# Performance work log

Hardware: AMD Instinct MI355X
Metric: run time of the kernel (lower is better)

Reference implementation:

```python
import jax, jax.numpy as jnp
import numpy as np
import math

H = 12   # num_attention_heads
DH = 64  # attention_head_size
D = H * DH  # hidden_size = 768


def _split_heads(x):
    # [b, s, D] -> [b, H, s, DH]
    b, s, _ = x.shape
    return x.reshape(b, s, H, DH).transpose(0, 2, 1, 3)


def setup_inputs() -> dict:
    key = jax.random.key(0)
    ks = jax.random.split(key, 8)
    B, S, G, NUM_CTX = 32, 512, 16, 8
    real_b = B // NUM_CTX
    inp = {
        "hidden_states": jax.random.normal(ks[0], (B, S, D), dtype=jnp.float32),
        "attention_mask": jnp.zeros((B, 1, 1, S), dtype=jnp.float32),
        "global_tokens_embed": jax.random.normal(ks[1], (real_b, G, D), dtype=jnp.float32),
        "Wq": jax.random.normal(ks[2], (D, D), dtype=jnp.float32) * 0.02,
        "bq": jnp.zeros((D,), dtype=jnp.float32),
        "Wk": jax.random.normal(ks[3], (D, D), dtype=jnp.float32) * 0.02,
        "bk": jnp.zeros((D,), dtype=jnp.float32),
        "Wv": jax.random.normal(ks[4], (D, D), dtype=jnp.float32) * 0.02,
        "bv": jnp.zeros((D,), dtype=jnp.float32),
        "num_ctx": 8,
    }
    return inp


def reference(hidden_states, attention_mask, global_tokens_embed,
              Wq, bq, Wk, bk, Wv, bv, num_ctx):
    B, S, _ = hidden_states.shape
    real_b = B // num_ctx
    G = global_tokens_embed.shape[1]
    scale = 1.0 / math.sqrt(DH)

    # Q/K/V projections for packed contexts
    q = _split_heads(hidden_states @ Wq + bq)   # [B,H,S,DH]
    k = _split_heads(hidden_states @ Wk + bk)
    v = _split_heads(hidden_states @ Wv + bv)

    # Global token projections
    gq = _split_heads(global_tokens_embed @ Wq + bq)  # [real_b,H,G,DH]
    gk = _split_heads(global_tokens_embed @ Wk + bk)
    gv = _split_heads(global_tokens_embed @ Wv + bv)

    # ---- Global-token cross attention over all contexts of each real batch ----
    # [B,H,S,DH] -> [real_b, H, num_ctx*S, DH]
    full_k = k.transpose(0, 2, 1, 3).reshape(real_b, num_ctx * S, H, DH).transpose(0, 2, 1, 3)
    full_v = v.transpose(0, 2, 1, 3).reshape(real_b, num_ctx * S, H, DH).transpose(0, 2, 1, 3)
    full_k = jnp.concatenate([gk, full_k], axis=2)  # [real_b,H,G+num_ctx*S,DH]
    full_v = jnp.concatenate([gv, full_v], axis=2)

    g_scores = jnp.einsum('bhgd,bhkd->bhgk', gq, full_k) * scale
    g_mask = attention_mask.reshape(real_b, num_ctx * S)[:, None, None, :]
    g_mask = jnp.concatenate([jnp.zeros((real_b, 1, 1, G), g_mask.dtype), g_mask], axis=3)
    g_scores = g_scores + g_mask
    g_probs = jax.nn.softmax(g_scores, axis=-1)
    g_ctx = jnp.einsum('bhgk,bhkd->bhgd', g_probs, full_v)
    g_ctx = g_ctx.transpose(0, 2, 1, 3).reshape(real_b, G, D)  # [real_b,G,D]

    # ---- Local attention: each context attends to its own tokens + global tokens ----
    gk_rep = jnp.broadcast_to(gk[:, None], (real_b, num_ctx, H, G, DH)).reshape(B, H, G, DH)
    gv_rep = jnp.broadcast_to(gv[:, None], (real_b, num_ctx, H, G, DH)).reshape(B, H, G, DH)
    k2 = jnp.concatenate([gk_rep, k], axis=2)  # [B,H,G+S,DH]
    v2 = jnp.concatenate([gv_rep, v], axis=2)
    mask2 = jnp.concatenate([jnp.zeros((B, 1, 1, G), attention_mask.dtype), attention_mask], axis=3)

    scores = jnp.einsum('bhqd,bhkd->bhqk', q, k2) * scale + mask2  # [B,H,S,G+S]
    probs = jax.nn.softmax(scores, axis=-1)
    ctx = jnp.einsum('bhqk,bhkd->bhqd', probs, v2)
    ctx = ctx.transpose(0, 2, 1, 3).reshape(B, S, D)  # [B,S,D]

    return ctx, g_ctx
```

## Files before the change

### kernel.cpp

```cpp
#include <hip/hip_runtime.h>
#include <hip/hip_bf16.h>
#include <stdint.h>

#define NH 12
#define DHD 64
#define DM 768
#define BB 32
#define SS 512
#define GG 16
#define NCTX 8
#define RBATCH 4
#define NSPLIT 16
#define OUTG_OFF ((size_t)BB * SS * DM)

#define XROWS 16512
#define NALL 2304
#define NX8 (XROWS * DM / 8)
#define NB8 (NALL / 8)
#define NM8 (BB * SS / 8)

#define LOG2E 1.4426950408889634f
#define QSCALE 0.18033688011112042f

typedef __bf16 bf16x8 __attribute__((ext_vector_type(8)));
typedef float f32x4 __attribute__((ext_vector_type(4)));
typedef float f32x16 __attribute__((ext_vector_type(16)));

__device__ __forceinline__ float b2f(unsigned short u) {
    union { unsigned int i; float f; } x;
    x.i = ((unsigned int)u) << 16;
    return x.f;
}
__device__ __forceinline__ unsigned short f2b(float f) {
    __hip_bfloat16 h = __float2bfloat16(f);
    return *reinterpret_cast<unsigned short*>(&h);
}
__device__ __forceinline__ unsigned int pk2(float a, float b) {
    return ((unsigned int)f2b(b) << 16) | (unsigned int)f2b(a);
}
__device__ __forceinline__ float ex2(float x) {
    return __builtin_amdgcn_exp2f(x);
}
__device__ __forceinline__ float ldv(const void* p, size_t i, int isf32) {
    return isf32 ? ((const float*)p)[i] : b2f(((const unsigned short*)p)[i]);
}
__device__ __forceinline__ void stv(void* p, size_t i, int isf32, float v) {
    if (isf32) ((float*)p)[i] = v;
    else       ((unsigned short*)p)[i] = f2b(v);
}
__device__ __forceinline__ void async_cp16(const unsigned short* g, unsigned short* l) {
    __builtin_amdgcn_global_load_lds(
        (const __attribute__((address_space(1))) unsigned int*)g,
        (__attribute__((address_space(3))) unsigned int*)l, 16, 0, 0);
}

__device__ __forceinline__ void vt_pair_store(unsigned int* Vt32, int vr, int scc,
                                              uint4 a, uint4 b, int ldq) {
    const unsigned int* au = (const unsigned int*)&a;
    const unsigned int* bu = (const unsigned int*)&b;
    #pragma unroll
    for (int i = 0; i < 4; i++) {
        const int d0 = scc + 2 * i;
        const int swz = ((vr >> 3) ^ ((d0 >> 3) & 7));
        const int i32 = d0 * ldq + (swz << 2) + ((vr & 7) >> 1);
        Vt32[i32]       = __builtin_amdgcn_perm(bu[i], au[i], 0x05040100u);
        Vt32[i32 + ldq] = __builtin_amdgcn_perm(bu[i], au[i], 0x07060302u);
    }
}

__global__ __launch_bounds__(256) void detect_dtype(
    const unsigned short* __restrict__ Wq, int* __restrict__ flag)
{
    __shared__ int hi, zz;
    if (threadIdx.x == 0) { hi = 0; zz = 0; }
    __syncthreads();
    int lh = 0, lz = 0;
    for (int i = threadIdx.x; i < 4096; i += 256) {
        unsigned short u = Wq[2 * i];
        if (((u >> 7) & 0xFF) >= 130) lh++;
        if (u == 0) lz++;
    }
    atomicAdd(&hi, lh);
    atomicAdd(&zz, lz);
    __syncthreads();
    if (threadIdx.x == 0) *flag = (hi > 512 || zz > 3500) ? 1 : 0;
}

__global__ __launch_bounds__(256) void cvt_x(
    const void* __restrict__ hs, const void* __restrict__ gte,
    const void* __restrict__ bq, const void* __restrict__ bk,
    const void* __restrict__ bv, const void* __restrict__ mask,
    const int* __restrict__ flag,
    unsigned short* __restrict__ Xb, unsigned short* __restrict__ b_all,
    unsigned short* __restrict__ wmask)
{
    const int e = blockIdx.x * 256 + threadIdx.x;
    const int isf32 = *flag;
    if (e < NX8) {
        const int base = e * 8;
        const int row = base / DM, col = base % DM;
        unsigned short o8[8];
        if (row < 16384) {
            if (isf32) {
                float4 a = ((const float4*)hs)[e * 2];
                float4 c = ((const float4*)hs)[e * 2 + 1];
                o8[0]=f2b(a.x); o8[1]=f2b(a.y); o8[2]=f2b(a.z); o8[3]=f2b(a.w);
                o8[4]=f2b(c.x); o8[5]=f2b(c.y); o8[6]=f2b(c.z); o8[7]=f2b(c.w);
            } else {
                *(uint4*)o8 = ((const uint4*)hs)[e];
            }
        } else if (row < 16448) {
            size_t soff = (size_t)(row - 16384) * DM + col;
            #pragma unroll
            for (int i = 0; i < 8; i++) o8[i] = f2b(ldv(gte, soff + i, isf32));
        } else {
            #pragma unroll
            for (int i = 0; i < 8; i++) o8[i] = 0;
        }
        *(uint4*)&Xb[base] = *(const uint4*)o8;
    } else if (e < NX8 + NB8) {
        const int i0 = (e - NX8) * 8;
        #pragma unroll
        for (int i = 0; i < 8; i++) {
            int ng = i0 + i;
            int z = ng / DM;
            const void* src = (z == 0) ? bq : (z == 1) ? bk : bv;
            b_all[ng] = f2b(ldv(src, ng % DM, isf32));
        }
    } else if (e < NX8 + NB8 + NM8) {
        const int i0 = (e - NX8 - NB8) * 8;
        #pragma unroll
        for (int i = 0; i < 8; i++)
            wmask[i0 + i] = f2b(ldv(mask, i0 + i, isf32) * LOG2E);
    }
}

__global__ __launch_bounds__(256) void cvt_w(
    const void* __restrict__ Wq, const void* __restrict__ Wk,
    const void* __restrict__ Wv, const int* __restrict__ flag,
    unsigned short* __restrict__ Wt)
{
    __shared__ float T[64][65];
    const int kt = blockIdx.x;
    const int ngt = blockIdx.y;
    const int z = ngt / 12, nt = ngt % 12;
    const int tid = threadIdx.x;
    const int isf32 = *flag;
    const void* W = (z == 0) ? Wq : (z == 1) ? Wk : Wv;

    for (int jj = 0; jj < 16; jj++) {
        int el = tid + jj * 256;
        int r = el >> 6, c = el & 63;
        T[r][c] = ldv(W, (size_t)(kt * 64 + r) * DM + nt * 64 + c, isf32);
    }
    __syncthreads();
    for (int jj = 0; jj < 16; jj++) {
        int el = tid + jj * 256;
        int rn = el >> 6, ck = el & 63;
        Wt[(size_t)(z * DM + nt * 64 + rn) * DM + kt * 64 + ck] = f2b(T[ck][rn]);
    }
}

#define QKV_NWG (129 * 18)
__global__ __launch_bounds__(256) void qkv_gemm(
    const unsigned short* __restrict__ Xb,
    const unsigned short* __restrict__ Wt,
    const unsigned short* __restrict__ b_all,
    unsigned short* __restrict__ q, unsigned short* __restrict__ kk_,
    unsigned short* __restrict__ v,
    unsigned short* __restrict__ gq, unsigned short* __restrict__ gk,
    unsigned short* __restrict__ gv)
{
    __shared__ __align__(16) unsigned short As[2][2][128 * 32];
    __shared__ __align__(16) unsigned short Bs[2][2][128 * 32];

    const int orig = blockIdx.x;
    const int q8 = QKV_NWG >> 3, r8 = QKV_NWG & 7;
    const int xcd = orig & 7, lin = orig >> 3;
    const int swz = (xcd < r8 ? xcd * (q8 + 1) : r8 * (q8 + 1) + (xcd - r8) * q8) + lin;
    const int mt = swz / 18, nt = swz - mt * 18;

    const int tid = threadIdx.x;
    const int wave = tid >> 6, lane = tid & 63;
    const int quad = lane >> 4, l16 = lane & 15;
    const int wm = wave & 1, wn = wave >> 1;
    const int z = nt / 6;
    unsigned short* YL = (z == 0) ? q : (z == 1) ? kk_ : v;
    unsigned short* YG = (z == 0) ? gq : (z == 1) ? gk : gv;
    const float qsc = (z == 0) ? QSCALE : 1.0f;

    const int sr = tid >> 2, sc = (tid & 3) * 8;

    const unsigned short* Arow0 = &Xb[(size_t)(mt * 128 + sr) * DM + sc];
    const unsigned short* Arow1 = Arow0 + (size_t)64 * DM;
    const unsigned short* Brow0 = &Wt[(size_t)(nt * 128 + sr) * DM + sc];
    const unsigned short* Brow1 = Brow0 + (size_t)64 * DM;

    f32x4 acc[4][4];
    #pragma unroll
    for (int i = 0; i < 4; i++)
        for (int j = 0; j < 4; j++)
            for (int r = 0; r < 4; r++) acc[i][j][r] = 0.f;

#define QKV_STAGE_PAIR(p, bb) do {                                       \
        const int k0_ = (p) * 64;                                        \
        async_cp16(Arow0 + k0_,      &As[(bb)][0][wave * 512]);          \
        async_cp16(Arow1 + k0_,      &As[(bb)][0][2048 + wave * 512]);   \
        async_cp16(Brow0 + k0_,      &Bs[(bb)][0][wave * 512]);          \
        async_cp16(Brow1 + k0_,      &Bs[(bb)][0][2048 + wave * 512]);   \
        async_cp16(Arow0 + k0_ + 32, &As[(bb)][1][wave * 512]);          \
        async_cp16(Arow1 + k0_ + 32, &As[(bb)][1][2048 + wave * 512]);   \
        async_cp16(Brow0 + k0_ + 32, &Bs[(bb)][1][wave * 512]);          \
        async_cp16(Brow1 + k0_ + 32, &Bs[(bb)][1][2048 + wave * 512]);   \
    } while (0)

    QKV_STAGE_PAIR(0, 0);
    __syncthreads();

    int cur = 0;
    for (int p = 0; p < 12; p++) {
        if (p < 11) QKV_STAGE_PAIR(p + 1, cur ^ 1);

        #pragma unroll
        for (int sub = 0; sub < 2; sub++) {
            bf16x8 af[4], bf[4];
            #pragma unroll
            for (int ib = 0; ib < 4; ib++)
                af[ib] = *(const bf16x8*)&As[cur][sub][(wm * 64 + ib * 16 + l16) * 32 + quad * 8];
            #pragma unroll
            for (int jb = 0; jb < 4; jb++)
                bf[jb] = *(const bf16x8*)&Bs[cur][sub][(wn * 64 + jb * 16 + l16) * 32 + quad * 8];
            #pragma unroll
            for (int ib = 0; ib < 4; ib++)
                #pragma unroll
                for (int jb = 0; jb < 4; jb++)
                    acc[ib][jb] = __builtin_amdgcn_mfma_f32_16x16x32_bf16(
                        bf[jb], af[ib], acc[ib][jb], 0, 0, 0);
        }

        if (p < 11) __syncthreads();
        cur ^= 1;
    }
#undef QKV_STAGE_PAIR

    #pragma unroll
    for (int ib = 0; ib < 4; ib++) {
        const int m = mt * 128 + wm * 64 + ib * 16 + l16;
        if (m >= 16448) continue;
        const bool loc = (m < 16384);
        const int b = m >> 9, s = m & 511;
        const int gl = m - 16384;
        const int rbx = gl >> 4, g = gl & 15;
        #pragma unroll
        for (int jb = 0; jb < 4; jb++) {
            const int ng0 = nt * 128 + wn * 64 + jb * 16 + quad * 4;
            const int o = ng0 - z * DM;
            const int h = o >> 6, dh0 = o & 63;
            const uint2 bu = *(const uint2*)&b_all[ng0];
            const unsigned short* bp = (const unsigned short*)&bu;
            const float y0 = (acc[ib][jb][0] + b2f(bp[0])) * qsc;
            const float y1 = (acc[ib][jb][1] + b2f(bp[1])) * qsc;
            const float y2 = (acc[ib][jb][2] + b2f(bp[2])) * qsc;
            const float y3 = (acc[ib][jb][3] + b2f(bp[3])) * qsc;
            uint2 o2;
            o2.x = pk2(y0, y1);
            o2.y = pk2(y2, y3);
            if (loc) {
                *(uint2*)&YL[(((size_t)b * NH + h) * SS + s) * DHD + dh0] = o2;
            } else {
                *(uint2*)&YG[(((size_t)rbx * NH + h) * GG + g) * DHD + dh0] = o2;
            }
        }
    }
}

#define AL_NWG (4 * NH * BB)
__global__ __launch_bounds__(256) void attn_local(
    const unsigned short* __restrict__ q,
    const unsigned short* __restrict__ k,
    const unsigned short* __restrict__ v,
    const unsigned short* __restrict__ gk,
    const unsigned short* __restrict__ gv,
    const unsigned short* __restrict__ wmask,
    const int* __restrict__ flag,
    void* __restrict__ out)
{
    __shared__ __align__(16) unsigned short Ks[2][64 * 64];
    __shared__ __align__(16) unsigned short Vt[2][64 * 64];

    const int orig = blockIdx.x;
    const int swz = (orig & 7) * (AL_NWG / 8) + (orig >> 3);
    const int qt = swz & 3;
    const int hb = swz >> 2;
    const int h = hb % NH, b = hb / NH;

    const int rb = b >> 3;
    const int tid = threadIdx.x, wave = tid >> 6, lane = tid & 63;
    const int l31 = lane & 31, h8 = lane >> 5;
    const int isf32 = *flag;
    const int q0 = qt * 128 + wave * 32;

    const size_t bh = (size_t)b * NH + h;
    const unsigned short* qp = q + bh * SS * DHD;
    const unsigned short* kp = k + bh * SS * DHD;
    const unsigned short* vp = v + bh * SS * DHD;
    const size_t gbh = (size_t)rb * NH + h;
    const unsigned short* gkp = gk + gbh * GG * DHD;
    const unsigned short* gvp = gv + gbh * GG * DHD;

    bf16x8 qf[4];
    #pragma unroll
    for (int kb = 0; kb < 4; kb++)
        qf[kb] = *(const bf16x8*)&qp[(size_t)(q0 + l31) * DHD + kb * 16 + h8 * 8];

    f32x16 oacc[2];
    #pragma unroll
    for (int mb = 0; mb < 2; mb++)
        #pragma unroll
        for (int j = 0; j < 16; j++) oacc[mb][j] = 0.f;
    float m_s = -1e30f, l_s = 0.f;

    const int sr = tid >> 3, scc = (tid & 7) * 8;
    const int vr = sr * 2;
    const int agc = (((lane & 7) ^ ((lane >> 3) & 7)) << 3);
    const int arow = 8 * wave + (lane >> 3);

    if (sr < 16) {
        uint4 kx = *(const uint4*)&gkp[sr * DHD + scc];
        *(uint4*)&Ks[0][sr * 64 + (((scc >> 3) ^ (sr & 7)) << 3)] = kx;
    } else {
        uint4 zz4 = {0, 0, 0, 0};
        *(uint4*)&Ks[0][sr * 64 + (((scc >> 3) ^ (sr & 7)) << 3)] = zz4;
    }
    {
        uint4 va0 = {0, 0, 0, 0}, vb0 = {0, 0, 0, 0};
        if (sr < 8) {
            va0 = *(const uint4*)&gvp[vr * DHD + scc];
            vb0 = *(const uint4*)&gvp[(vr + 1) * DHD + scc];
        }
        vt_pair_store((unsigned int*)Vt[0], vr, scc, va0, vb0, 32);
    }
    __syncthreads();

    for (int t = 0; t < 9; t++) {
        const int cur = t & 1;
        const unsigned short* KsC = Ks[cur];
        const unsigned short* VtC = Vt[cur];

        uint4 va, vb;
        if (t < 8) {
            const int ks0 = t * 64;
            va = *(const uint4*)&vp[(size_t)(ks0 + vr) * DHD + scc];
            vb = *(const uint4*)&vp[(size_t)(ks0 + vr + 1) * DHD + scc];
            #pragma unroll
            for (int p = 0; p < 2; p++)
                async_cp16(&kp[(size_t)(ks0 + p * 32 + arow) * DHD + agc],
                           &Ks[cur ^ 1][p * 2048 + wave * 512]);
        }

        f32x16 scA, scB;
        #pragma unroll
        for (int kt = 0; kt < 2; kt++) {
            f32x16 cc;
            #pragma unroll
            for (int j = 0; j < 16; j++) cc[j] = 0.f;
            if (kt == 0 || t > 0) {
                #pragma unroll
                for (int kb = 0; kb < 4; kb++) {
                    const int key = kt * 32 + l31;
                    bf16x8 kf = *(const bf16x8*)&KsC[key * 64 + (((kb * 2 + h8) ^ (key & 7)) << 3)];
                    cc = __builtin_amdgcn_mfma_f32_32x32x16_bf16(kf, qf[kb], cc, 0, 0, 0);
                }
                if (t > 0) {
                    #pragma unroll
                    for (int rg = 0; rg < 4; rg++) {
                        uint2 mu = *(const uint2*)&wmask[b * SS + (t - 1) * 64 + kt * 32 + rg * 8 + 4 * h8];
                        const unsigned short* mp = (const unsigned short*)&mu;
                        #pragma unroll
                        for (int r = 0; r < 4; r++)
                            cc[rg * 4 + r] += b2f(mp[r]);
                    }
                } else {
                    #pragma unroll
                    for (int j = 8; j < 16; j++) cc[j] = -1e30f;
                }
            } else {
                #pragma unroll
                for (int j = 0; j < 16; j++) cc[j] = -1e30f;
            }
            if (kt == 0) scA = cc; else scB = cc;
        }

        float mx = -1e30f;
        #pragma unroll
        for (int j = 0; j < 16; j++) mx = fmaxf(mx, scA[j]);
        #pragma unroll
        for (int j = 0; j < 16; j++) mx = fmaxf(mx, scB[j]);
        mx = fmaxf(mx, __shfl_xor(mx, 32, 64));
        if (!__all(mx <= m_s)) {
            const float mn = fmaxf(m_s, mx);
            const float alpha = ex2(m_s - mn);
            m_s = mn;
            l_s *= alpha;
            #pragma unroll
            for (int mb = 0; mb < 2; mb++)
                #pragma unroll
                for (int j = 0; j < 16; j++) oacc[mb][j] *= alpha;
        }
        float rs = 0.f;
        #pragma unroll
        for (int j = 0; j < 16; j++) { float pw = ex2(scA[j] - m_s); scA[j] = pw; rs += pw; }
        #pragma unroll
        for (int j = 0; j < 16; j++) { float pw = ex2(scB[j] - m_s); scB[j] = pw; rs += pw; }
        rs += __shfl_xor(rs, 32, 64);
        l_s += rs;

        #pragma unroll
        for (int kt = 0; kt < 2; kt++) {
            unsigned int wA[4], wB[4];
            #pragma unroll
            for (int g = 0; g < 4; g++) {
                const float s0 = (kt == 0) ? scA[4 * g + 0] : scB[4 * g + 0];
                const float s1 = (kt == 0) ? scA[4 * g + 1] : scB[4 * g + 1];
                const float s2 = (kt == 0) ? scA[4 * g + 2] : scB[4 * g + 2];
                const float s3 = (kt == 0) ? scA[4 * g + 3] : scB[4 * g + 3];
                wA[g] = pk2(s0, s1);
                wB[g] = pk2(s2, s3);
            }
            #pragma unroll
            for (int kb = 0; kb < 2; kb++) {
                auto ra  = __builtin_amdgcn_permlane32_swap(wA[2 * kb], wA[2 * kb + 1], false, false);
                auto rbp = __builtin_amdgcn_permlane32_swap(wB[2 * kb], wB[2 * kb + 1], false, false);
                union { unsigned int u[4]; bf16x8 v8; } pfu;
                pfu.u[0] = (unsigned int)ra[0];
                pfu.u[1] = (unsigned int)rbp[0];
                pfu.u[2] = (unsigned int)ra[1];
                pfu.u[3] = (unsigned int)rbp[1];
                const int kb2 = kt * 2 + kb;
                #pragma unroll
                for (int mb = 0; mb < 2; mb++) {
                    const int d = mb * 32 + l31;
                    bf16x8 vf = *(const bf16x8*)&VtC[d * 64 + (((kb2 * 2 + h8) ^ ((d >> 3) & 7)) << 3)];
                    oacc[mb] = __builtin_amdgcn_mfma_f32_32x32x16_bf16(vf, pfu.v8, oacc[mb], 0, 0, 0);
                }
            }
        }

        if (t < 8) {
            vt_pair_store((unsigned int*)Vt[cur ^ 1], vr, scc, va, vb, 32);
            __syncthreads();
        }
    }

    const float inv = 1.f / l_s;
    const int s = q0 + l31;
    #pragma unroll
    for (int mb = 0; mb < 2; mb++) {
        #pragma unroll
        for (int rg = 0; rg < 4; rg++) {
            const int d0 = mb * 32 + rg * 8 + 4 * h8;
            const size_t idx = ((size_t)b * SS + s) * DM + h * DHD + d0;
            if (isf32) {
                float4 o4;
                o4.x = oacc[mb][rg * 4 + 0] * inv;
                o4.y = oacc[mb][rg * 4 + 1] * inv;
                o4.z = oacc[mb][rg * 4 + 2] * inv;
                o4.w = oacc[mb][rg * 4 + 3] * inv;
                *(float4*)&((float*)out)[idx] = o4;
            } else {
                uint2 o2;
                o2.x = pk2(oacc[mb][rg * 4 + 0] * inv, oacc[mb][rg * 4 + 1] * inv);
                o2.y = pk2(oacc[mb][rg * 4 + 2] * inv, oacc[mb][rg * 4 + 3] * inv);
                *(uint2*)&((unsigned short*)out)[idx] = o2;
            }
        }
    }
}

__global__ __launch_bounds__(256) void attn_gsplit(
    const unsigned short* __restrict__ k,
    const unsigned short* __restrict__ v,
    const unsigned short* __restrict__ gq,
    const unsigned short* __restrict__ gk,
    const unsigned short* __restrict__ gv,
    const unsigned short* __restrict__ wmask,
    float* __restrict__ Opart, float* __restrict__ Mpart,
    float* __restrict__ Lpart)
{
    __shared__ __align__(16) unsigned short Ks[128 * 64];
    __shared__ __align__(16) unsigned short Vt[64 * 128];
    __shared__ __align__(16) unsigned short Ps[4 * 16 * 64];

    const int h = blockIdx.x, rb = blockIdx.y, sp = blockIdx.z;
    const int tid = threadIdx.x, wave = tid >> 6, lane = tid & 63;
    const int quad = lane >> 4, l16 = lane & 15;

    const size_t gbh = (size_t)rb * NH + h;
    const unsigned short* gqp = gq + gbh * GG * DHD;
    const unsigned short* gkp = gk + gbh * GG * DHD;
    const unsigned short* gvp = gv + gbh * GG * DHD;

    bf16x8 aq[2];
    aq[0] = *(const bf16x8*)&gqp[l16 * DHD + quad * 8];
    aq[1] = *(const bf16x8*)&gqp[l16 * DHD + 32 + quad * 8];

    f32x4 oacc[4];
    #pragma unroll
    for (int db = 0; db < 4; db++)
        for (int r = 0; r < 4; r++) oacc[db][r] = 0.f;
    float m_s = -1e30f, l_s = 0.f;

    const int sr = tid >> 3, scc = (tid & 7) * 8;
    const int vr = sr * 2;
    const int agc = (((lane & 7) ^ ((lane >> 3) & 7)) << 3);
    const int arow = 8 * wave + (lane >> 3);
    unsigned short* myP = &Ps[wave * 1024];
    unsigned int* Vt32 = (unsigned int*)Vt;

    const int nt = (sp == 0) ? 3 : 2;
    for (int ti = 0; ti < nt; ti++) {
        const bool gtile = (sp == 0 && ti == 0);
        int cb = 0, soff = 0;
        __syncthreads();
        if (gtile) {
            if (sr < 16) {
                uint4 kx = *(const uint4*)&gkp[sr * DHD + scc];
                *(uint4*)&Ks[sr * 64 + (((scc >> 3) ^ (sr & 7)) << 3)] = kx;
                uint4 va = {0, 0, 0, 0}, vb = {0, 0, 0, 0};
                if (sr < 8) {
                    va = *(const uint4*)&gvp[vr * DHD + scc];
                    vb = *(const uint4*)&gvp[(vr + 1) * DHD + scc];
                }
                vt_pair_store(Vt32, vr, scc, va, vb, 64);
            } else {
                uint4 zz4 = {0, 0, 0, 0};
                *(uint4*)&Ks[sr * 64 + (((scc >> 3) ^ (sr & 7)) << 3)] = zz4;
            }
        } else {
            const int kidx = sp * 256 + (ti - ((sp == 0) ? 1 : 0)) * 128;
            cb = rb * NCTX + (kidx >> 9);
            soff = kidx & 511;
            const unsigned short* kp = k + ((size_t)cb * NH + h) * SS * DHD;
            const unsigned short* vp = v + ((size_t)cb * NH + h) * SS * DHD;
            #pragma unroll
            for (int p = 0; p < 4; p++)
                async_cp16(&kp[(size_t)(soff + p * 32 + arow) * DHD + agc],
                           &Ks[p * 2048 + wave * 512]);
            #pragma unroll
            for (int pp = 0; pp < 2; pp++) {
                const int vrr = vr + pp * 64;
                uint4 va = *(const uint4*)&vp[(size_t)(soff + vrr) * DHD + scc];
                uint4 vb = *(const uint4*)&vp[(size_t)(soff + vrr + 1) * DHD + scc];
                vt_pair_store(Vt32, vrr, scc, va, vb, 64);
            }
        }
        __syncthreads();

        if (gtile && wave != 0) continue;

        const int nbn = gtile ? 1 : 2;
        f32x4 c[2];
        for (int hh = 0; hh < nbn; hh++) {
            f32x4 cc = {0.f, 0.f, 0.f, 0.f};
            const int key = wave * 32 + hh * 16 + l16;
            #pragma unroll
            for (int kd = 0; kd < 2; kd++) {
                bf16x8 kf = *(const bf16x8*)&Ks[key * 64 + (((kd * 4 + quad) ^ (key & 7)) << 3)];
                cc = __builtin_amdgcn_mfma_f32_16x16x32_bf16(kf, aq[kd], cc, 0, 0, 0);
            }
            if (!gtile) {
                uint2 mu = *(const uint2*)&wmask[cb * SS + soff + wave * 32 + hh * 16 + quad * 4];
                const unsigned short* mp = (const unsigned short*)&mu;
                #pragma unroll
                for (int r = 0; r < 4; r++)
                    cc[r] += b2f(mp[r]);
            }
            c[hh] = cc;
        }

        float mx = -1e30f;
        for (int hh = 0; hh < nbn; hh++)
            #pragma unroll
            for (int r = 0; r < 4; r++) mx = fmaxf(mx, c[hh][r]);
        mx = fmaxf(mx, __shfl_xor(mx, 16, 64));
        mx = fmaxf(mx, __shfl_xor(mx, 32, 64));
        const float mn = fmaxf(m_s, mx);
        const float alpha = ex2(m_s - mn);
        m_s = mn;
        float rs = 0.f;
        for (int hh = 0; hh < nbn; hh++)
            #pragma unroll
            for (int r = 0; r < 4; r++) {
                float p = ex2(c[hh][r] - mn);
                c[hh][r] = p;
                rs += p;
            }
        rs += __shfl_xor(rs, 16, 64);
        rs += __shfl_xor(rs, 32, 64);
        l_s = l_s * alpha + rs;
        #pragma unroll
        for (int db = 0; db < 4; db++)
            for (int r = 0; r < 4; r++) oacc[db][r] *= alpha;

        for (int hh = 0; hh < nbn; hh++) {
            uint2 pw;
            pw.x = pk2(c[hh][0], c[hh][1]);
            pw.y = pk2(c[hh][2], c[hh][3]);
            const int cch = ((hh * 2 + (quad >> 1)) ^ (l16 & 7));
            *(uint2*)&myP[l16 * 64 + cch * 8 + (quad & 1) * 4] = pw;
        }
        if (nbn == 1) {
            uint2 zz2; zz2.x = 0; zz2.y = 0;
            const int cch = ((2 + (quad >> 1)) ^ (l16 & 7));
            *(uint2*)&myP[l16 * 64 + cch * 8 + (quad & 1) * 4] = zz2;
        }

        bf16x8 pf = *(const bf16x8*)&myP[l16 * 64 + ((quad ^ (l16 & 7)) << 3)];
        #pragma unroll
        for (int db = 0; db < 4; db++) {
            const int d = db * 16 + l16;
            const int kc = wave * 4 + quad;
            bf16x8 vf = *(const bf16x8*)&Vt[d * 128 + ((kc ^ ((d >> 3) & 7)) << 3)];
            oacc[db] = __builtin_amdgcn_mfma_f32_16x16x32_bf16(vf, pf, oacc[db], 0, 0, 0);
        }
    }

    __syncthreads();
    float* Om = (float*)Ks;
    float* Mw = (float*)Vt;
    float* Lw = Mw + 64;
    #pragma unroll
    for (int db = 0; db < 4; db++)
        for (int r = 0; r < 4; r++)
            Om[(wave * 16 + l16) * 64 + db * 16 + quad * 4 + r] = oacc[db][r];
    if (quad == 0) {
        Mw[wave * 16 + l16] = m_s;
        Lw[wave * 16 + l16] = l_s;
    }
    __syncthreads();

    const size_t pbase = ((size_t)(sp * RBATCH + rb) * NH + h) * 1024;
    for (int e = tid; e < 1024; e += 256) {
        const int qrow = e >> 6, d = e & 63;
        float M = fmaxf(fmaxf(Mw[qrow], Mw[16 + qrow]), fmaxf(Mw[32 + qrow], Mw[48 + qrow]));
        float acc = 0.f, L = 0.f;
        #pragma unroll
        for (int w = 0; w < 4; w++) {
            float scw = ex2(Mw[w * 16 + qrow] - M);
            acc += Om[(w * 16 + qrow) * 64 + d] * scw;
            L += Lw[w * 16 + qrow] * scw;
        }
        Opart[pbase + e] = acc;
        if (d == 0) {
            Mpart[((sp * RBATCH + rb) * NH + h) * 16 + qrow] = M;
            Lpart[((sp * RBATCH + rb) * NH + h) * 16 + qrow] = L;
        }
    }
}

__global__ __launch_bounds__(256) void attn_gmerge(
    const float* __restrict__ Opart, const float* __restrict__ Mpart,
    const float* __restrict__ Lpart, const int* __restrict__ flag,
    void* __restrict__ out)
{
    const int h = blockIdx.x, rb = blockIdx.y;
    const int tid = threadIdx.x;
    const int isf32 = *flag;
    for (int e = tid; e < 1024; e += 256) {
        const int qrow = e >> 6, d = e & 63;
        float M = -1e30f;
        #pragma unroll
        for (int sp = 0; sp < NSPLIT; sp++)
            M = fmaxf(M, Mpart[((sp * RBATCH + rb) * NH + h) * 16 + qrow]);
        float acc = 0.f, L = 0.f;
        #pragma unroll
        for (int sp = 0; sp < NSPLIT; sp++) {
            const size_t pb = ((size_t)(sp * RBATCH + rb) * NH + h);
            float scs = ex2(Mpart[pb * 16 + qrow] - M);
            acc += Opart[pb * 1024 + e] * scs;
            L += Lpart[pb * 16 + qrow] * scs;
        }
        stv(out, OUTG_OFF + ((size_t)rb * GG + qrow) * DM + h * DHD + d, isf32, acc / L);
    }
}

extern "C" void kernel_launch(void* const* d_in, const int* in_sizes, int n_in,
                              void* d_out, int out_size, void* d_ws, size_t ws_size,
                              hipStream_t stream) {
    const void* hs   = d_in[0];
    const void* mask = d_in[1];
    const void* gte  = d_in[2];
    const void* Wq   = d_in[3];
    const void* bq   = d_in[4];
    const void* Wk   = d_in[5];
    const void* bk   = d_in[6];
    const void* Wv   = d_in[7];
    const void* bv   = d_in[8];

    const size_t qkv_sz = (size_t)BB * NH * SS * DHD;
    const size_t g_sz   = (size_t)RBATCH * NH * GG * DHD;
    const size_t msk_sz = (size_t)BB * SS;
    const size_t x_sz   = (size_t)XROWS * DM;
    const size_t wt_sz  = (size_t)NALL * DM;
    const size_t ba_sz  = (size_t)NALL;
    const size_t need_hw = 3 * qkv_sz + 3 * g_sz + msk_sz + x_sz + wt_sz + ba_sz;
    if (ws_size < need_hw * 2 + 16) return;

    unsigned short* q     = (unsigned short*)d_ws;
    unsigned short* kk    = q + qkv_sz;
    unsigned short* vv    = kk + qkv_sz;
    unsigned short* gq    = vv + qkv_sz;
    unsigned short* gk    = gq + g_sz;
    unsigned short* gv    = gk + g_sz;
    unsigned short* wmask = gv + g_sz;
    unsigned short* Xb    = wmask + msk_sz;
    unsigned short* Wt    = Xb + x_sz;
    unsigned short* b_all = Wt + wt_sz;
    int* flag = (int*)(b_all + ba_sz);
    float* Opart = (float*)Xb;
    float* Mpart = Opart + (size_t)NSPLIT * RBATCH * NH * 1024;
    float* Lpart = Mpart + (size_t)NSPLIT * RBATCH * NH * 16;

    detect_dtype<<<1, 256, 0, stream>>>((const unsigned short*)Wq, flag);

    const int cvt_items = NX8 + NB8 + NM8;
    cvt_x<<<(cvt_items + 255) / 256, 256, 0, stream>>>(
        hs, gte, bq, bk, bv, mask, flag, Xb, b_all, wmask);
    cvt_w<<<dim3(12, 36), 256, 0, stream>>>(Wq, Wk, Wv, flag, Wt);

    qkv_gemm<<<dim3(QKV_NWG), 256, 0, stream>>>(Xb, Wt, b_all, q, kk, vv, gq, gk, gv);

    attn_local<<<dim3(AL_NWG), 256, 0, stream>>>(
        q, kk, vv, gk, gv, wmask, flag, d_out);
    attn_gsplit<<<dim3(NH, RBATCH, NSPLIT), 256, 0, stream>>>(
        kk, vv, gq, gk, gv, wmask, Opart, Mpart, Lpart);
    attn_gmerge<<<dim3(NH, RBATCH), 256, 0, stream>>>(
        Opart, Mpart, Lpart, flag, d_out);
}
```

Measured before the change: 349.5 us.

## Fuse global split attention into local attention kernel launch and reduce split count

Merges the global-token split-attention kernel into the local attention kernel as extra leading workgroups, dispatched by block index, so both run in a single launch sharing one LDS buffer. It also cuts the global split count from 16 to 4, so each global block processes 8 key tiles instead of 2. This removes one kernel launch and lets the global blocks overlap with local work. In exchange the long-running global blocks may become a tail, and the shared LDS size is now the larger of the two footprints, which could lower occupancy for the local path. A redundant duplicated macro definition is also introduced and then immediately redefined.

```diff
diff --git a/kernel.cpp b/kernel.cpp
--- a/kernel.cpp
+++ b/kernel.cpp
@@ -10,7 +10,7 @@
 #define GG 16
 #define NCTX 8
 #define RBATCH 4
-#define NSPLIT 16
+#define NSPLIT 4
 #define OUTG_OFF ((size_t)BB * SS * DM)
 
 #define XROWS 16512
@@ -207,6 +207,14 @@
         async_cp16(Arow0 + k0_,      &As[(bb)][0][wave * 512]);          \
         async_cp16(Arow1 + k0_,      &As[(bb)][0][2048 + wave * 512]);   \
         async_cp16(Brow0 + k0_,      &Bs[(bb)][0][wave * 512]);          \
+        async_cp16(Brow0 + k0_,      &Bs[(bb)][0][wave * 512]);          \
+    } while (0)
+#undef QKV_STAGE_PAIR
+#define QKV_STAGE_PAIR(p, bb) do {                                       \
+        const int k0_ = (p) * 64;                                        \
+        async_cp16(Arow0 + k0_,      &As[(bb)][0][wave * 512]);          \
+        async_cp16(Arow1 + k0_,      &As[(bb)][0][2048 + wave * 512]);   \
+        async_cp16(Brow0 + k0_,      &Bs[(bb)][0][wave * 512]);          \
         async_cp16(Brow1 + k0_,      &Bs[(bb)][0][2048 + wave * 512]);   \
         async_cp16(Arow0 + k0_ + 32, &As[(bb)][1][wave * 512]);          \
         async_cp16(Arow1 + k0_ + 32, &As[(bb)][1][2048 + wave * 512]);   \
@@ -274,28 +282,211 @@
     }
 }
 
+#define GS_NWG (NH * RBATCH * NSPLIT)
 #define AL_NWG (4 * NH * BB)
-__global__ __launch_bounds__(256) void attn_local(
+__global__ __launch_bounds__(256) void attn_fused(
     const unsigned short* __restrict__ q,
     const unsigned short* __restrict__ k,
     const unsigned short* __restrict__ v,
+    const unsigned short* __restrict__ gq,
     const unsigned short* __restrict__ gk,
     const unsigned short* __restrict__ gv,
     const unsigned short* __restrict__ wmask,
     const int* __restrict__ flag,
-    void* __restrict__ out)
+    void* __restrict__ out,
+    float* __restrict__ Opart, float* __restrict__ Mpart,
+    float* __restrict__ Lpart)
 {
-    __shared__ __align__(16) unsigned short Ks[2][64 * 64];
-    __shared__ __align__(16) unsigned short Vt[2][64 * 64];
-
-    const int orig = blockIdx.x;
+    __shared__ __align__(16) unsigned short SMEM[20480];
+
+    const int tid = threadIdx.x, wave = tid >> 6, lane = tid & 63;
+    const int sr = tid >> 3, scc = (tid & 7) * 8;
+    const int vr = sr * 2;
+    const int agc = (((lane & 7) ^ ((lane >> 3) & 7)) << 3);
+    const int arow = 8 * wave + (lane >> 3);
+
+    if (blockIdx.x < GS_NWG) {
+        unsigned short* Ks = SMEM;
+        unsigned short* Vt = SMEM + 8192;
+        unsigned short* Ps = SMEM + 16384;
+        unsigned int* Vt32 = (unsigned int*)Vt;
+
+        const int idx = blockIdx.x;
+        const int h = idx % NH;
+        const int rb = (idx / NH) % RBATCH;
+        const int sp = idx / (NH * RBATCH);
+        const int quad = lane >> 4, l16 = lane & 15;
+
+        const size_t gbh = (size_t)rb * NH + h;
+        const unsigned short* gqp = gq + gbh * GG * DHD;
+        const unsigned short* gkp = gk + gbh * GG * DHD;
+        const unsigned short* gvp = gv + gbh * GG * DHD;
+
+        bf16x8 aq[2];
+        aq[0] = *(const bf16x8*)&gqp[l16 * DHD + quad * 8];
+        aq[1] = *(const bf16x8*)&gqp[l16 * DHD + 32 + quad * 8];
+
+        f32x4 oacc[4];
+        #pragma unroll
+        for (int db = 0; db < 4; db++)
+            for (int r = 0; r < 4; r++) oacc[db][r] = 0.f;
+        float m_s = -1e30f, l_s = 0.f;
+
+        unsigned short* myP = &Ps[wave * 1024];
+
+        const int ntt = (sp == 0) ? 9 : 8;
+        for (int ti = 0; ti < ntt; ti++) {
+            const bool gtile = (sp == 0 && ti == 0);
+            int cb = 0, soff = 0;
+            __syncthreads();
+            if (gtile) {
+                if (sr < 16) {
+                    uint4 kx = *(const uint4*)&gkp[sr * DHD + scc];
+                    *(uint4*)&Ks[sr * 64 + (((scc >> 3) ^ (sr & 7)) << 3)] = kx;
+                    uint4 va = {0, 0, 0, 0}, vb = {0, 0, 0, 0};
+                    if (sr < 8) {
+                        va = *(const uint4*)&gvp[vr * DHD + scc];
+                        vb = *(const uint4*)&gvp[(vr + 1) * DHD + scc];
+                    }
+                    vt_pair_store(Vt32, vr, scc, va, vb, 64);
+                } else {
+                    uint4 zz4 = {0, 0, 0, 0};
+                    *(uint4*)&Ks[sr * 64 + (((scc >> 3) ^ (sr & 7)) << 3)] = zz4;
+                }
+            } else {
+                const int kidx = sp * 1024 + (ti - ((sp == 0) ? 1 : 0)) * 128;
+                cb = rb * NCTX + (kidx >> 9);
+                soff = kidx & 511;
+                const unsigned short* kp = k + ((size_t)cb * NH + h) * SS * DHD;
+                const unsigned short* vp = v + ((size_t)cb * NH + h) * SS * DHD;
+                #pragma unroll
+                for (int p = 0; p < 4; p++)
+                    async_cp16(&kp[(size_t)(soff + p * 32 + arow) * DHD + agc],
+                               &Ks[p * 2048 + wave * 512]);
+                #pragma unroll
+                for (int pp = 0; pp < 2; pp++) {
+                    const int vrr = vr + pp * 64;
+                    uint4 va = *(const uint4*)&vp[(size_t)(soff + vrr) * DHD + scc];
+                    uint4 vb = *(const uint4*)&vp[(size_t)(soff + vrr + 1) * DHD + scc];
+                    vt_pair_store(Vt32, vrr, scc, va, vb, 64);
+                }
+            }
+            __syncthreads();
+
+            if (gtile && wave != 0) continue;
+
+            const int nbn = gtile ? 1 : 2;
+            f32x4 c[2];
+            for (int hh = 0; hh < nbn; hh++) {
+                f32x4 cc = {0.f, 0.f, 0.f, 0.f};
+                const int key = wave * 32 + hh * 16 + l16;
+                #pragma unroll
+                for (int kd = 0; kd < 2; kd++) {
+                    bf16x8 kf = *(const bf16x8*)&Ks[key * 64 + (((kd * 4 + quad) ^ (key & 7)) << 3)];
+                    cc = __builtin_amdgcn_mfma_f32_16x16x32_bf16(kf, aq[kd], cc, 0, 0, 0);
+                }
+                if (!gtile) {
+                    uint2 mu = *(const uint2*)&wmask[cb * SS + soff + wave * 32 + hh * 16 + quad * 4];
+                    const unsigned short* mp = (const unsigned short*)&mu;
+                    #pragma unroll
+                    for (int r = 0; r < 4; r++)
+                        cc[r] += b2f(mp[r]);
+                }
+                c[hh] = cc;
+            }
+
+            float mx = -1e30f;
+            for (int hh = 0; hh < nbn; hh++)
+                #pragma unroll
+                for (int r = 0; r < 4; r++) mx = fmaxf(mx, c[hh][r]);
+            mx = fmaxf(mx, __shfl_xor(mx, 16, 64));
+            mx = fmaxf(mx, __shfl_xor(mx, 32, 64));
+            const float mn = fmaxf(m_s, mx);
+            const float alpha = ex2(m_s - mn);
+            m_s = mn;
+            float rs = 0.f;
+            for (int hh = 0; hh < nbn; hh++)
+                #pragma unroll
+                for (int r = 0; r < 4; r++) {
+                    float p = ex2(c[hh][r] - mn);
+                    c[hh][r] = p;
+                    rs += p;
+                }
+            rs += __shfl_xor(rs, 16, 64);
+            rs += __shfl_xor(rs, 32, 64);
+            l_s = l_s * alpha + rs;
+            #pragma unroll
+            for (int db = 0; db < 4; db++)
+                for (int r = 0; r < 4; r++) oacc[db][r] *= alpha;
+
+            for (int hh = 0; hh < nbn; hh++) {
+                uint2 pw;
+                pw.x = pk2(c[hh][0], c[hh][1]);
+                pw.y = pk2(c[hh][2], c[hh][3]);
+                const int cch = ((hh * 2 + (quad >> 1)) ^ (l16 & 7));
+                *(uint2*)&myP[l16 * 64 + cch * 8 + (quad & 1) * 4] = pw;
+            }
+            if (nbn == 1) {
+                uint2 zz2; zz2.x = 0; zz2.y = 0;
+                const int cch = ((2 + (quad >> 1)) ^ (l16 & 7));
+                *(uint2*)&myP[l16 * 64 + cch * 8 + (quad & 1) * 4] = zz2;
+            }
+
+            bf16x8 pf = *(const bf16x8*)&myP[l16 * 64 + ((quad ^ (l16 & 7)) << 3)];
+            #pragma unroll
+            for (int db = 0; db < 4; db++) {
+                const int d = db * 16 + l16;
+                const int kc = wave * 4 + quad;
+                bf16x8 vf = *(const bf16x8*)&Vt[d * 128 + ((kc ^ ((d >> 3) & 7)) << 3)];
+                oacc[db] = __builtin_amdgcn_mfma_f32_16x16x32_bf16(vf, pf, oacc[db], 0, 0, 0);
+            }
+        }
+
+        __syncthreads();
+        float* Om = (float*)Ks;
+        float* Mw = (float*)Vt;
+        float* Lw = Mw + 64;
+        const int quad2 = lane >> 4, l162 = lane & 15;
+        #pragma unroll
+        for (int db = 0; db < 4; db++)
+            for (int r = 0; r < 4; r++)
+                Om[(wave * 16 + l162) * 64 + db * 16 + quad2 * 4 + r] = oacc[db][r];
+        if (quad2 == 0) {
+            Mw[wave * 16 + l162] = m_s;
+            Lw[wave * 16 + l162] = l_s;
+        }
+        __syncthreads();
+
+        const size_t pbase = ((size_t)(sp * RBATCH + rb) * NH + h) * 1024;
+        for (int e = tid; e < 1024; e += 256) {
+            const int qrow = e >> 6, d = e & 63;
+            float M = fmaxf(fmaxf(Mw[qrow], Mw[16 + qrow]), fmaxf(Mw[32 + qrow], Mw[48 + qrow]));
+            float acc = 0.f, L = 0.f;
+            #pragma unroll
+            for (int w = 0; w < 4; w++) {
+                float scw = ex2(Mw[w * 16 + qrow] - M);
+                acc += Om[(w * 16 + qrow) * 64 + d] * scw;
+                L += Lw[w * 16 + qrow] * scw;
+            }
+            Opart[pbase + e] = acc;
+            if (d == 0) {
+                Mpart[((sp * RBATCH + rb) * NH + h) * 16 + qrow] = M;
+                Lpart[((sp * RBATCH + rb) * NH + h) * 16 + qrow] = L;
+            }
+        }
+        return;
+    }
+
+    unsigned short* KsBuf = SMEM;
+    unsigned short* VtBuf = SMEM + 8192;
+
+    const int orig = blockIdx.x - GS_NWG;
     const int swz = (orig & 7) * (AL_NWG / 8) + (orig >> 3);
     const int qt = swz & 3;
     const int hb = swz >> 2;
     const int h = hb % NH, b = hb / NH;
 
     const int rb = b >> 3;
-    const int tid = threadIdx.x, wave = tid >> 6, lane = tid & 63;
     const int l31 = lane & 31, h8 = lane >> 5;
     const int isf32 = *flag;
     const int q0 = qt * 128 + wave * 32;
@@ -320,17 +511,12 @@
         for (int j = 0; j < 16; j++) oacc[mb][j] = 0.f;
     float m_s = -1e30f, l_s = 0.f;
 
-    const int sr = tid >> 3, scc = (tid & 7) * 8;
-    const int vr = sr * 2;
-    const int agc = (((lane & 7) ^ ((lane >> 3) & 7)) << 3);
-    const int arow = 8 * wave + (lane >> 3);
-
     if (sr < 16) {
         uint4 kx = *(const uint4*)&gkp[sr * DHD + scc];
-        *(uint4*)&Ks[0][sr * 64 + (((scc >> 3) ^ (sr & 7)) << 3)] = kx;
+        *(uint4*)&KsBuf[sr * 64 + (((scc >> 3) ^ (sr & 7)) << 3)] = kx;
     } else {
         uint4 zz4 = {0, 0, 0, 0};
-        *(uint4*)&Ks[0][sr * 64 + (((scc >> 3) ^ (sr & 7)) << 3)] = zz4;
+        *(uint4*)&KsBuf[sr * 64 + (((scc >> 3) ^ (sr & 7)) << 3)] = zz4;
     }
     {
         uint4 va0 = {0, 0, 0, 0}, vb0 = {0, 0, 0, 0};
@@ -338,14 +524,14 @@
             va0 = *(const uint4*)&gvp[vr * DHD + scc];
             vb0 = *(const uint4*)&gvp[(vr + 1) * DHD + scc];
         }
-        vt_pair_store((unsigned int*)Vt[0], vr, scc, va0, vb0, 32);
+        vt_pair_store((unsigned int*)VtBuf, vr, scc, va0, vb0, 32);
     }
     __syncthreads();
 
     for (int t = 0; t < 9; t++) {
         const int cur = t & 1;
-        const unsigned short* KsC = Ks[cur];
-        const unsigned short* VtC = Vt[cur];
+        const unsigned short* KsC = KsBuf + cur * 4096;
+        const unsigned short* VtC = VtBuf + cur * 4096;
 
         uint4 va, vb;
         if (t < 8) {
@@ -355,7 +541,7 @@
             #pragma unroll
             for (int p = 0; p < 2; p++)
                 async_cp16(&kp[(size_t)(ks0 + p * 32 + arow) * DHD + agc],
-                           &Ks[cur ^ 1][p * 2048 + wave * 512]);
+                           &KsBuf[(cur ^ 1) * 4096 + p * 2048 + wave * 512]);
         }
 
         f32x16 scA, scB;
@@ -447,7 +633,7 @@
         }
 
         if (t < 8) {
-            vt_pair_store((unsigned int*)Vt[cur ^ 1], vr, scc, va, vb, 32);
+            vt_pair_store((unsigned int*)(VtBuf + (cur ^ 1) * 4096), vr, scc, va, vb, 32);
             __syncthreads();
         }
     }
@@ -477,187 +663,6 @@
     }
 }
 
-__global__ __launch_bounds__(256) void attn_gsplit(
-    const unsigned short* __restrict__ k,
-    const unsigned short* __restrict__ v,
-    const unsigned short* __restrict__ gq,
-    const unsigned short* __restrict__ gk,
-    const unsigned short* __restrict__ gv,
-    const unsigned short* __restrict__ wmask,
-    float* __restrict__ Opart, float* __restrict__ Mpart,
-    float* __restrict__ Lpart)
-{
-    __shared__ __align__(16) unsigned short Ks[128 * 64];
-    __shared__ __align__(16) unsigned short Vt[64 * 128];
-    __shared__ __align__(16) unsigned short Ps[4 * 16 * 64];
-
-    const int h = blockIdx.x, rb = blockIdx.y, sp = blockIdx.z;
-    const int tid = threadIdx.x, wave = tid >> 6, lane = tid & 63;
-    const int quad = lane >> 4, l16 = lane & 15;
-
-    const size_t gbh = (size_t)rb * NH + h;
-    const unsigned short* gqp = gq + gbh * GG * DHD;
-    const unsigned short* gkp = gk + gbh * GG * DHD;
-    const unsigned short* gvp = gv + gbh * GG * DHD;
-
-    bf16x8 aq[2];
-    aq[0] = *(const bf16x8*)&gqp[l16 * DHD + quad * 8];
-    aq[1] = *(const bf16x8*)&gqp[l16 * DHD + 32 + quad * 8];
-
-    f32x4 oacc[4];
-    #pragma unroll
-    for (int db = 0; db < 4; db++)
-        for (int r = 0; r < 4; r++) oacc[db][r] = 0.f;
-    float m_s = -1e30f, l_s = 0.f;
-
-    const int sr = tid >> 3, scc = (tid & 7) * 8;
-    const int vr = sr * 2;
-    const int agc = (((lane & 7) ^ ((lane >> 3) & 7)) << 3);
-    const int arow = 8 * wave + (lane >> 3);
-    unsigned short* myP = &Ps[wave * 1024];
-    unsigned int* Vt32 = (unsigned int*)Vt;
-
-    const int nt = (sp == 0) ? 3 : 2;
-    for (int ti = 0; ti < nt; ti++) {
-        const bool gtile = (sp == 0 && ti == 0);
-        int cb = 0, soff = 0;
-        __syncthreads();
-        if (gtile) {
-            if (sr < 16) {
-                uint4 kx = *(const uint4*)&gkp[sr * DHD + scc];
-                *(uint4*)&Ks[sr * 64 + (((scc >> 3) ^ (sr & 7)) << 3)] = kx;
-                uint4 va = {0, 0, 0, 0}, vb = {0, 0, 0, 0};
-                if (sr < 8) {
-                    va = *(const uint4*)&gvp[vr * DHD + scc];
-                    vb = *(const uint4*)&gvp[(vr + 1) * DHD + scc];
-                }
-                vt_pair_store(Vt32, vr, scc, va, vb, 64);
-            } else {
-                uint4 zz4 = {0, 0, 0, 0};
-                *(uint4*)&Ks[sr * 64 + (((scc >> 3) ^ (sr & 7)) << 3)] = zz4;
-            }
-        } else {
-            const int kidx = sp * 256 + (ti - ((sp == 0) ? 1 : 0)) * 128;
-            cb = rb * NCTX + (kidx >> 9);
-            soff = kidx & 511;
-            const unsigned short* kp = k + ((size_t)cb * NH + h) * SS * DHD;
-            const unsigned short* vp = v + ((size_t)cb * NH + h) * SS * DHD;
-            #pragma unroll
-            for (int p = 0; p < 4; p++)
-                async_cp16(&kp[(size_t)(soff + p * 32 + arow) * DHD + agc],
-                           &Ks[p * 2048 + wave * 512]);
-            #pragma unroll
-            for (int pp = 0; pp < 2; pp++) {
-                const int vrr = vr + pp * 64;
-                uint4 va = *(const uint4*)&vp[(size_t)(soff + vrr) * DHD + scc];
-                uint4 vb = *(const uint4*)&vp[(size_t)(soff + vrr + 1) * DHD + scc];
-                vt_pair_store(Vt32, vrr, scc, va, vb, 64);
-            }
-        }
-        __syncthreads();
-
-        if (gtile && wave != 0) continue;
-
-        const int nbn = gtile ? 1 : 2;
-        f32x4 c[2];
-        for (int hh = 0; hh < nbn; hh++) {
-            f32x4 cc = {0.f, 0.f, 0.f, 0.f};
-            const int key = wave * 32 + hh * 16 + l16;
-            #pragma unroll
-            for (int kd = 0; kd < 2; kd++) {
-                bf16x8 kf = *(const bf16x8*)&Ks[key * 64 + (((kd * 4 + quad) ^ (key & 7)) << 3)];
-                cc = __builtin_amdgcn_mfma_f32_16x16x32_bf16(kf, aq[kd], cc, 0, 0, 0);
-            }
-            if (!gtile) {
-                uint2 mu = *(const uint2*)&wmask[cb * SS + soff + wave * 32 + hh * 16 + quad * 4];
-                const unsigned short* mp = (const unsigned short*)&mu;
-                #pragma unroll
-                for (int r = 0; r < 4; r++)
-                    cc[r] += b2f(mp[r]);
-            }
-            c[hh] = cc;
-        }
-
-        float mx = -1e30f;
-        for (int hh = 0; hh < nbn; hh++)
-            #pragma unroll
-            for (int r = 0; r < 4; r++) mx = fmaxf(mx, c[hh][r]);
-        mx = fmaxf(mx, __shfl_xor(mx, 16, 64));
-        mx = fmaxf(mx, __shfl_xor(mx, 32, 64));
-        const float mn = fmaxf(m_s, mx);
-        const float alpha = ex2(m_s - mn);
-        m_s = mn;
-        float rs = 0.f;
-        for (int hh = 0; hh < nbn; hh++)
-            #pragma unroll
-            for (int r = 0; r < 4; r++) {
-                float p = ex2(c[hh][r] - mn);
-                c[hh][r] = p;
-                rs += p;
-            }
-        rs += __shfl_xor(rs, 16, 64);
-        rs += __shfl_xor(rs, 32, 64);
-        l_s = l_s * alpha + rs;
-        #pragma unroll
-        for (int db = 0; db < 4; db++)
-            for (int r = 0; r < 4; r++) oacc[db][r] *= alpha;
-
-        for (int hh = 0; hh < nbn; hh++) {
-            uint2 pw;
-            pw.x = pk2(c[hh][0], c[hh][1]);
-            pw.y = pk2(c[hh][2], c[hh][3]);
-            const int cch = ((hh * 2 + (quad >> 1)) ^ (l16 & 7));
-            *(uint2*)&myP[l16 * 64 + cch * 8 + (quad & 1) * 4] = pw;
-        }
-        if (nbn == 1) {
-            uint2 zz2; zz2.x = 0; zz2.y = 0;
-            const int cch = ((2 + (quad >> 1)) ^ (l16 & 7));
-            *(uint2*)&myP[l16 * 64 + cch * 8 + (quad & 1) * 4] = zz2;
-        }
-
-        bf16x8 pf = *(const bf16x8*)&myP[l16 * 64 + ((quad ^ (l16 & 7)) << 3)];
-        #pragma unroll
-        for (int db = 0; db < 4; db++) {
-            const int d = db * 16 + l16;
-            const int kc = wave * 4 + quad;
-            bf16x8 vf = *(const bf16x8*)&Vt[d * 128 + ((kc ^ ((d >> 3) & 7)) << 3)];
-            oacc[db] = __builtin_amdgcn_mfma_f32_16x16x32_bf16(vf, pf, oacc[db], 0, 0, 0);
-        }
-    }
-
-    __syncthreads();
-    float* Om = (float*)Ks;
-    float* Mw = (float*)Vt;
-    float* Lw = Mw + 64;
-    #pragma unroll
-    for (int db = 0; db < 4; db++)
-        for (int r = 0; r < 4; r++)
-            Om[(wave * 16 + l16) * 64 + db * 16 + quad * 4 + r] = oacc[db][r];
-    if (quad == 0) {
-        Mw[wave * 16 + l16] = m_s;
-        Lw[wave * 16 + l16] = l_s;
-    }
-    __syncthreads();
-
-    const size_t pbase = ((size_t)(sp * RBATCH + rb) * NH + h) * 1024;
-    for (int e = tid; e < 1024; e += 256) {
-        const int qrow = e >> 6, d = e & 63;
-        float M = fmaxf(fmaxf(Mw[qrow], Mw[16 + qrow]), fmaxf(Mw[32 + qrow], Mw[48 + qrow]));
-        float acc = 0.f, L = 0.f;
-        #pragma unroll
-        for (int w = 0; w < 4; w++) {
-            float scw = ex2(Mw[w * 16 + qrow] - M);
-            acc += Om[(w * 16 + qrow) * 64 + d] * scw;
-            L += Lw[w * 16 + qrow] * scw;
-        }
-        Opart[pbase + e] = acc;
-        if (d == 0) {
-            Mpart[((sp * RBATCH + rb) * NH + h) * 16 + qrow] = M;
-            Lpart[((sp * RBATCH + rb) * NH + h) * 16 + qrow] = L;
-        }
-    }
-}
-
 __global__ __launch_bounds__(256) void attn_gmerge(
     const float* __restrict__ Opart, const float* __restrict__ Mpart,
     const float* __restrict__ Lpart, const int* __restrict__ flag,
@@ -730,10 +735,8 @@
 
     qkv_gemm<<<dim3(QKV_NWG), 256, 0, stream>>>(Xb, Wt, b_all, q, kk, vv, gq, gk, gv);
 
-    attn_local<<<dim3(AL_NWG), 256, 0, stream>>>(
-        q, kk, vv, gk, gv, wmask, flag, d_out);
-    attn_gsplit<<<dim3(NH, RBATCH, NSPLIT), 256, 0, stream>>>(
-        kk, vv, gq, gk, gv, wmask, Opart, Mpart, Lpart);
+    attn_fused<<<dim3(GS_NWG + AL_NWG), 256, 0, stream>>>(
+        q, kk, vv, gq, gk, gv, wmask, flag, d_out, Opart, Mpart, Lpart);
     attn_gmerge<<<dim3(NH, RBATCH), 256, 0, stream>>>(
         Opart, Mpart, Lpart, flag, d_out);
 }
```

After: 316.9 us. -9.3%, faster.
